# Optimization experiments

Measured on AMD Instinct MI355X. Metric: run time of the kernel, lower is better.

The kernel has to match this reference:

```python
import jax, jax.numpy as jnp
import numpy as np

B, T, D = 2, 2048, 1024
QH, KVH = 16, 4
HD = D // QH          # 64
G = QH // KVH         # group size 4
SCALE = HD ** -0.5


def _rope_rotate(x):
    # interleaved rotation: (x1, x2) -> (-x2, x1)
    x1 = x[..., ::2]
    x2 = x[..., 1::2]
    return jnp.stack((-x2, x1), axis=-1).reshape(x.shape)


def setup_inputs() -> dict:
    key = jax.random.key(0)
    k0, k1, k2, k3 = jax.random.split(key, 4)
    x = jax.random.normal(k0, (B, T, D), dtype=jnp.float32)
    # proper RoPE tables, shape [T, HD], each frequency repeated for the interleaved pair
    inv_freq = 1.0 / (10000.0 ** (np.arange(0, HD, 2, dtype=np.float32) / HD))
    freqs = np.arange(T, dtype=np.float32)[:, None] * inv_freq[None, :]   # [T, HD/2]
    freqs = np.repeat(freqs, 2, axis=-1)                                   # [T, HD]
    cos = jnp.asarray(np.cos(freqs), dtype=jnp.float32)
    sin = jnp.asarray(np.sin(freqs), dtype=jnp.float32)
    # glorot-uniform weights stored torch-style as [out, in]
    def glorot(k, out_d, in_d):
        lim = float(np.sqrt(6.0 / (in_d + out_d)))
        return jax.random.uniform(k, (out_d, in_d), jnp.float32, -lim, lim)
    Wq = glorot(k1, D, D)
    Wkv = glorot(k2, 2 * KVH * HD, D)
    Wo = glorot(k3, D, D)
    return {"x": x, "cos": cos, "sin": sin, "Wq": Wq, "Wkv": Wkv, "Wo": Wo}


def reference(x, cos, sin, Wq, Wkv, Wo):
    # projections (torch Linear: y = x @ W.T)
    q = (x @ Wq.T).reshape(B, T, QH, HD).transpose(0, 2, 1, 3)        # [B,QH,T,HD]
    kv = (x @ Wkv.T).reshape(B, T, KVH, 2, HD)
    k = kv[..., 0, :].transpose(0, 2, 1, 3)                            # [B,KVH,T,HD]
    v = kv[..., 1, :].transpose(0, 2, 1, 3)                            # [B,KVH,T,HD]
    # inline RoPE (cos/sin broadcast over batch & heads)
    q = q * cos + _rope_rotate(q) * sin
    k = k * cos + _rope_rotate(k) * sin
    # GQA via broadcast instead of repeat_interleave (same math)
    qg = q.reshape(B, KVH, G, T, HD)
    scores = jnp.einsum('bkgtd,bksd->bkgts', qg, k) * SCALE            # [B,KVH,G,T,T]
    attn = jax.nn.softmax(scores, axis=-1)  # dropout is identity in eval
    out = jnp.einsum('bkgts,bksd->bkgtd', attn, v)                     # [B,KVH,G,T,HD]
    out = out.reshape(B, QH, T, HD).transpose(0, 2, 1, 3).reshape(B, T, D)
    return out @ Wo.T
```

## Files before the change

kernel.cpp:

```cpp
#include <hip/hip_runtime.h>


typedef __bf16 bf16x8 __attribute__((ext_vector_type(8)));
typedef float f32x4 __attribute__((ext_vector_type(4)));
typedef float f32x16 __attribute__((ext_vector_type(16)));
typedef int i32x4 __attribute__((ext_vector_type(4)));
typedef unsigned short ushort4v __attribute__((ext_vector_type(4)));
typedef unsigned short ushort8v __attribute__((ext_vector_type(8)));
typedef unsigned short u16;
typedef unsigned int u32;

#define DEVINL __device__ __forceinline__

DEVINL float bf2f(u16 u) {
  unsigned int x = ((unsigned int)u) << 16;
  return __builtin_bit_cast(float, x);
}
DEVINL u16 f2bf(float f) {
  unsigned int x = __builtin_bit_cast(unsigned int, f);
  x += 0x7fffu + ((x >> 16) & 1u);
  return (u16)(x >> 16);
}
DEVINL float exp2r(float x) {
  float r;
  asm("v_exp_f32 %0, %1" : "=v"(r) : "v"(x));
  return r;
}

constexpr int Bb = 2, Tt = 2048, Dd = 1024, QH = 16, KVH = 4, HD = 64;
constexpr float SCALE_L2E = 0.125f * 1.44269504088896340736f;
constexpr int KVSZ = 131072;

__global__ void cvt_all(const float* __restrict__ x, const float* __restrict__ Wq,
                        const float* __restrict__ Wkv, const float* __restrict__ Wo,
                        u16* __restrict__ xb, u16* __restrict__ wqkv,
                        u16* __restrict__ wob) {
  int i = blockIdx.x * 256 + threadIdx.x;
  const float* src;
  u16* dst;
  if (i < 1048576) {
    src = x; dst = xb;
  } else if (i < 1310720) {
    src = Wq - (size_t)1048576 * 4; dst = wqkv - (size_t)1048576 * 4;
  } else if (i < 1441792) {
    src = Wkv - (size_t)1310720 * 4; dst = wqkv + (size_t)1024 * 1024 - (size_t)1310720 * 4;
  } else {
    src = Wo - (size_t)1441792 * 4; dst = wob - (size_t)1441792 * 4;
  }
  float4 v = reinterpret_cast<const float4*>(src)[i];
  ushort4v o = {f2bf(v.x), f2bf(v.y), f2bf(v.z), f2bf(v.w)};
  *reinterpret_cast<ushort4v*>(dst + (size_t)i * 4) = o;
}

template <bool OUT_F32, int BNF>
__global__ __launch_bounds__(256) void gemm_bt(const u16* __restrict__ A,
                                               const u16* __restrict__ Bw,
                                               void* __restrict__ Cout, int M, int N, int K) {
  __shared__ alignas(16) u16 lA[128 * 64];
  __shared__ alignas(16) u16 lB[BNF * 32 * 64];
  const int tid = threadIdx.x;
  const int w = tid >> 6, lane = tid & 63;
  const int r16 = lane & 15, g4 = lane >> 4;
  const int row0 = blockIdx.y * 128, col0 = blockIdx.x * (BNF * 32);
  const int sr = tid >> 3, sc = tid & 7;
  const int NT = K >> 6;

  bf16x8 ra[4], rb[BNF];
  f32x4 acc[4][BNF];
#pragma unroll
  for (int i = 0; i < 4; ++i)
#pragma unroll
    for (int j = 0; j < BNF; ++j) acc[i][j] = f32x4{0.f, 0.f, 0.f, 0.f};

  const int wm = (w >> 1) * 64, wn = (w & 1) * (BNF * 8);

#pragma unroll
  for (int i = 0; i < 4; ++i) {
    int r = i * 32 + sr;
    ra[i] = *reinterpret_cast<const bf16x8*>(A + (size_t)(row0 + r) * K + sc * 8);
  }
#pragma unroll
  for (int i = 0; i < BNF; ++i) {
    int r = i * 32 + sr;
    rb[i] = *reinterpret_cast<const bf16x8*>(Bw + (size_t)(col0 + r) * K + sc * 8);
  }

  for (int kt = 0; kt < NT; ++kt) {
    __syncthreads();
#pragma unroll
    for (int i = 0; i < 4; ++i) {
      int r = i * 32 + sr;
      int c = (sc ^ (r & 7)) * 8;
      *reinterpret_cast<bf16x8*>(&lA[r * 64 + c]) = ra[i];
    }
#pragma unroll
    for (int i = 0; i < BNF; ++i) {
      int r = i * 32 + sr;
      int c = (sc ^ (r & 7)) * 8;
      *reinterpret_cast<bf16x8*>(&lB[r * 64 + c]) = rb[i];
    }
    __syncthreads();
    if (kt + 1 < NT) {
      int k0 = (kt + 1) << 6;
#pragma unroll
      for (int i = 0; i < 4; ++i) {
        int r = i * 32 + sr;
        ra[i] = *reinterpret_cast<const bf16x8*>(A + (size_t)(row0 + r) * K + k0 + sc * 8);
      }
#pragma unroll
      for (int i = 0; i < BNF; ++i) {
        int r = i * 32 + sr;
        rb[i] = *reinterpret_cast<const bf16x8*>(Bw + (size_t)(col0 + r) * K + k0 + sc * 8);
      }
    }
#pragma unroll
    for (int kk = 0; kk < 2; ++kk) {
      bf16x8 af[4], bfr[BNF];
#pragma unroll
      for (int mf = 0; mf < 4; ++mf) {
        int r = wm + mf * 16 + r16;
        int c = ((kk * 4 + g4) ^ (r & 7)) * 8;
        af[mf] = *reinterpret_cast<const bf16x8*>(&lA[r * 64 + c]);
      }
#pragma unroll
      for (int nf = 0; nf < BNF; ++nf) {
        int r = wn * 2 + nf * 16 + r16;
        int c = ((kk * 4 + g4) ^ (r & 7)) * 8;
        bfr[nf] = *reinterpret_cast<const bf16x8*>(&lB[r * 64 + c]);
      }
#pragma unroll
      for (int mf = 0; mf < 4; ++mf)
#pragma unroll
        for (int nf = 0; nf < BNF; ++nf)
          acc[mf][nf] =
              __builtin_amdgcn_mfma_f32_16x16x32_bf16(af[mf], bfr[nf], acc[mf][nf], 0, 0, 0);
    }
  }

#pragma unroll
  for (int mf = 0; mf < 4; ++mf)
#pragma unroll
    for (int nf = 0; nf < BNF; ++nf)
#pragma unroll
      for (int r = 0; r < 4; ++r) {
        size_t row = (size_t)(row0 + wm + mf * 16 + g4 * 4 + r);
        size_t col = (size_t)(col0 + wn * 2 + nf * 16 + r16);
        float v = acc[mf][nf][r];
        if (OUT_F32)
          reinterpret_cast<float*>(Cout)[row * N + col] = v;
        else
          reinterpret_cast<u16*>(Cout)[row * N + col] = f2bf(v);
      }
}

__global__ void rope_vt(const u16* __restrict__ P, const float* __restrict__ cosT,
                        const float* __restrict__ sinT, u16* __restrict__ Q,
                        u16* __restrict__ Kc, u16* __restrict__ Vf) {
  __shared__ u16 tile[64][72];
  const int bid = blockIdx.x;
  const int tid = threadIdx.x;
  if (bid < 10240) {
    int idx = bid * 256 + tid;
    int row = idx / 640, p = idx - row * 640;
    int b = row >> 11, t = row & 2047;
    int n, d;
    u16* outp;
    float scl;
    if (p < 512) {
      n = p * 2;
      int h = n >> 6;
      d = n & 63;
      outp = Q + ((size_t)(b * QH + h) * Tt + t) * HD + d;
      scl = SCALE_L2E;
    } else {
      int r2 = p - 512;
      int kvh = r2 >> 5, dp = r2 & 31;
      d = dp * 2;
      n = 1024 + kvh * 128 + d;
      int bh = b * KVH + kvh;
      int kf = d >> 4, h8 = (d >> 3) & 1, j = d & 7;
      outp = Kc + (size_t)bh * KVSZ + ((t >> 5) * 4 + kf) * 512 + (h8 * 32 + (t & 31)) * 8 + j;
      scl = 1.0f;
    }
    unsigned int pv = *reinterpret_cast<const unsigned int*>(P + (size_t)row * 1536 + n);
    float v0 = bf2f((u16)(pv & 0xffffu)), v1 = bf2f((u16)(pv >> 16));
    float c = cosT[t * HD + d], s = sinT[t * HD + d];
    float o0 = (v0 * c - v1 * s) * scl;
    float o1 = (v1 * c + v0 * s) * scl;
    unsigned int ob = (unsigned int)f2bf(o0) | ((unsigned int)f2bf(o1) << 16);
    *reinterpret_cast<unsigned int*>(outp) = ob;
  } else {
    int rem = bid - 10240;
    int bh = rem >> 5, tt = rem & 31;
    int b = bh >> 2, kvh = bh & 3;
    int t0 = tt * 64;
    int colbase = 1024 + kvh * 128 + 64;
#pragma unroll
    for (int j = 0; j < 4; ++j) {
      int rr = j * 16 + (tid >> 4);
      int cc = (tid & 15) * 4;
      *reinterpret_cast<uint2*>(&tile[rr][cc]) =
          *reinterpret_cast<const uint2*>(P + (size_t)(b * Tt + t0 + rr) * 1536 + colbase + cc);
    }
    __syncthreads();
#pragma unroll
    for (int kk = 0; kk < 2; ++kk) {
      int CH = kk * 256 + tid;
      int df = CH >> 8, sbks = (CH >> 6) & 3, h8 = (CH >> 5) & 1, l = CH & 31;
      int d = df * 32 + l;
      int c = (sbks >> 1) * 4 + (sbks & 1) * 2 + h8;
      ushort8v v;
#pragma unroll
      for (int j = 0; j < 8; ++j) v[j] = tile[c * 8 + j][d];
      u16* dst = Vf + (size_t)bh * KVSZ + (((t0 >> 6) * 2 + df) * 4 + sbks) * 512 +
                 (h8 * 32 + l) * 8;
      *reinterpret_cast<ushort8v*>(dst) = v;
    }
  }
}

__global__ __launch_bounds__(512, 4) void attn_fwd9(const u16* __restrict__ Q,
                                                    const u16* __restrict__ Kf,
                                                    const u16* __restrict__ Vf,
                                                    u16* __restrict__ Oa) {
  __shared__ alignas(16) float cmb[2][32][66];
  __shared__ alignas(16) u16 ot[2][32][72];
  const int tid = threadIdx.x;
  const int w = tid >> 6, lane = tid & 63;
  const int qsub = w & 1, spl = w >> 1;
  const int l31 = lane & 31, hi = lane >> 5;

  const int fid = blockIdx.x;
  const int xcd = fid & 7, idx = fid >> 3;
  const int b = xcd >> 2, kvh = xcd & 3;
  const int g = idx & 3, qblk = idx >> 2;
  const int h = kvh * 4 + g;
  const int t0 = qblk * 64 + qsub * 32;

  const u16* Qh = Q + ((size_t)(b * QH + h) * Tt + t0 + l31) * HD + hi * 8;
  const u16* Kp = Kf + (size_t)(b * KVH + kvh) * KVSZ + lane * 8 + (size_t)spl * 32768;
  const u16* Vp = Vf + (size_t)(b * KVH + kvh) * KVSZ + lane * 8 + (size_t)spl * 32768;

  bf16x8 qf[4];
#pragma unroll
  for (int kf = 0; kf < 4; ++kf)
    qf[kf] = *reinterpret_cast<const bf16x8*>(Qh + kf * 16);

  f32x16 oacc[2];
#pragma unroll
  for (int df = 0; df < 2; ++df)
#pragma unroll
    for (int r = 0; r < 16; ++r) oacc[df][r] = 0.f;
  float lp = 0.f;

  for (int it = 0; it < 8; ++it, Kp += 4096, Vp += 4096) {
    bf16x8 kfr[2][4];
#pragma unroll
    for (int sb = 0; sb < 2; ++sb)
#pragma unroll
      for (int kf = 0; kf < 4; ++kf)
        kfr[sb][kf] = *reinterpret_cast<const bf16x8*>(Kp + sb * 2048 + kf * 512);

    f32x16 sacc[2];
#pragma unroll
    for (int sb = 0; sb < 2; ++sb)
#pragma unroll
      for (int r = 0; r < 16; ++r) sacc[sb][r] = 0.f;
    __builtin_amdgcn_s_setprio(1);
#pragma unroll
    for (int sb = 0; sb < 2; ++sb)
#pragma unroll
      for (int kf = 0; kf < 4; ++kf)
        sacc[sb] = __builtin_amdgcn_mfma_f32_32x32x16_bf16(kfr[sb][kf], qf[kf], sacc[sb], 0, 0, 0);
    __builtin_amdgcn_s_setprio(0);

    bf16x8 vf[2][2][2];
#pragma unroll
    for (int df = 0; df < 2; ++df)
#pragma unroll
      for (int sb = 0; sb < 2; ++sb)
#pragma unroll
        for (int ks = 0; ks < 2; ++ks)
          vf[df][sb][ks] =
              *reinterpret_cast<const bf16x8*>(Vp + (size_t)(df * 4 + sb * 2 + ks) * 512);

    float a0 = 0.f, a1 = 0.f, a2 = 0.f, a3 = 0.f;
#pragma unroll
    for (int sb = 0; sb < 2; ++sb)
#pragma unroll
      for (int r = 0; r < 16; r += 4) {
        float e0 = exp2r(sacc[sb][r]);
        float e1 = exp2r(sacc[sb][r + 1]);
        float e2 = exp2r(sacc[sb][r + 2]);
        float e3 = exp2r(sacc[sb][r + 3]);
        sacc[sb][r] = e0; sacc[sb][r + 1] = e1; sacc[sb][r + 2] = e2; sacc[sb][r + 3] = e3;
        a0 += e0; a1 += e1; a2 += e2; a3 += e3;
      }
    lp += (a0 + a1) + (a2 + a3);

    bf16x8 pf[2][2];
#pragma unroll
    for (int sb = 0; sb < 2; ++sb) {
      u32 pw[8];
#pragma unroll
      for (int r2 = 0; r2 < 8; ++r2) {
        u32 o;
        asm("v_cvt_pk_bf16_f32 %0, %1, %2"
            : "=v"(o)
            : "v"(sacc[sb][2 * r2]), "v"(sacc[sb][2 * r2 + 1]));
        pw[r2] = o;
      }
      u32 fw[2][4];
#pragma unroll
      for (int pp = 0; pp < 4; ++pp) {
        int ks = pp >> 1, o = pp & 1;
        u32 a = pw[ks * 4 + o], bq = pw[ks * 4 + o + 2];
        asm("v_permlane32_swap_b32 %0, %1" : "+v"(a), "+v"(bq));
        fw[ks][o] = a;
        fw[ks][o + 2] = bq;
      }
#pragma unroll
      for (int ks = 0; ks < 2; ++ks) {
        i32x4 iv = {(int)fw[ks][0], (int)fw[ks][1], (int)fw[ks][2], (int)fw[ks][3]};
        pf[sb][ks] = __builtin_bit_cast(bf16x8, iv);
      }
    }

    __builtin_amdgcn_s_setprio(1);
#pragma unroll
    for (int df = 0; df < 2; ++df)
#pragma unroll
      for (int sb = 0; sb < 2; ++sb)
#pragma unroll
        for (int ks = 0; ks < 2; ++ks)
          oacc[df] =
              __builtin_amdgcn_mfma_f32_32x32x16_bf16(vf[df][sb][ks], pf[sb][ks], oacc[df], 0, 0, 0);
    __builtin_amdgcn_s_setprio(0);
  }

  lp += __shfl_xor(lp, 32);

  for (int src = 1; src < 4; ++src) {
    if (spl == src) {
      float* cb = &cmb[qsub][l31][0];
#pragma unroll
      for (int df = 0; df < 2; ++df)
#pragma unroll
        for (int r = 0; r < 16; ++r) {
          int d = df * 32 + (r & 3) + 8 * (r >> 2) + 4 * hi;
          cb[d] = oacc[df][r];
        }
      if (hi == 0) cb[64] = lp;
    }
    __syncthreads();
    if (spl == 0) {
      const float* cb = &cmb[qsub][l31][0];
      lp += cb[64];
#pragma unroll
      for (int df = 0; df < 2; ++df)
#pragma unroll
        for (int r = 0; r < 16; ++r) {
          int d = df * 32 + (r & 3) + 8 * (r >> 2) + 4 * hi;
          oacc[df][r] += cb[d];
        }
    }
    __syncthreads();
  }

  if (spl == 0) {
    float linv = 1.0f / lp;
#pragma unroll
    for (int df = 0; df < 2; ++df)
#pragma unroll
      for (int r = 0; r < 16; ++r) {
        int d = df * 32 + (r & 3) + 8 * (r >> 2) + 4 * hi;
        ot[qsub][l31][d] = f2bf(oacc[df][r] * linv);
      }
  }
  __syncthreads();
  if (spl == 0) {
    int tr = lane >> 1, dblk = (lane & 1) * 32;
    u16* gdst = Oa + ((size_t)(b * Tt + t0 + tr)) * Dd + h * HD + dblk;
#pragma unroll
    for (int c = 0; c < 4; ++c) {
      ushort8v vv = *reinterpret_cast<const ushort8v*>(&ot[qsub][tr][dblk + c * 8]);
      *reinterpret_cast<ushort8v*>(gdst + c * 8) = vv;
    }
  }
}

extern "C" void kernel_launch(void* const* d_in, const int* in_sizes, int n_in, void* d_out,
                              int out_size, void* d_ws, size_t ws_size, hipStream_t stream) {
  (void)in_sizes; (void)n_in; (void)out_size; (void)ws_size;
  const float* x = (const float*)d_in[0];
  const float* cosT = (const float*)d_in[1];
  const float* sinT = (const float*)d_in[2];
  const float* Wq = (const float*)d_in[3];
  const float* Wkv = (const float*)d_in[4];
  const float* Wo = (const float*)d_in[5];

  char* p = (char*)d_ws;
  u16* xb = (u16*)p;   p += (size_t)4096 * 1024 * 2;
  u16* wqkv = (u16*)p; p += (size_t)1536 * 1024 * 2;
  u16* wob = (u16*)p;  p += (size_t)1024 * 1024 * 2;
  u16* Pbuf = (u16*)p; p += (size_t)4096 * 1536 * 2;
  u16* Qb = (u16*)p;   p += (size_t)Bb * QH * Tt * HD * 2;
  u16* Kbuf = (u16*)p; p += (size_t)Bb * KVH * Tt * HD * 2;
  u16* Vfb = (u16*)p;  p += (size_t)Bb * KVH * HD * Tt * 2;
  u16* Ob = Pbuf;

  cvt_all<<<6656, 256, 0, stream>>>(x, Wq, Wkv, Wo, xb, wqkv, wob);
  gemm_bt<false, 4><<<dim3(12, 32), 256, 0, stream>>>(xb, wqkv, Pbuf, 4096, 1536, 1024);
  rope_vt<<<10496, 256, 0, stream>>>(Pbuf, cosT, sinT, Qb, Kbuf, Vfb);
  attn_fwd9<<<1024, 512, 0, stream>>>(Qb, Kbuf, Vfb, Ob);
  gemm_bt<true, 2><<<dim3(16, 32), 256, 0, stream>>>(Ob, wob, d_out, 4096, 1024, 1024);
}
```

Before: 107.4 us.

## Share K/V tiles across GQA heads via double-buffered LDS with async global-to-LDS loads

The attention kernel now handles all four query heads of a KV group in one block, with one wave per head per KV-split, and halves the grid. K and V tiles are staged into a double-buffered LDS arena using global_load_lds and shared by those heads, instead of each wave loading its own K/V from global memory. The KV split drops from four ways to two, so the cross-wave reduction runs once instead of three times. In exchange it adds a block-wide barrier per iteration, 64KB of LDS per block that may limit occupancy, and twice as many serial iterations per wave.

```diff
diff --git a/kernel.cpp b/kernel.cpp
--- a/kernel.cpp
+++ b/kernel.cpp
@@ -25,6 +25,11 @@
   float r;
   asm("v_exp_f32 %0, %1" : "=v"(r) : "v"(x));
   return r;
+}
+DEVINL void gld16(const u16* g, u16* l) {
+  __builtin_amdgcn_global_load_lds(
+      (const __attribute__((address_space(1))) void*)g,
+      (__attribute__((address_space(3))) void*)l, 16, 0, 0);
 }
 
 constexpr int Bb = 2, Tt = 2048, Dd = 1024, QH = 16, KVH = 4, HD = 64;
@@ -219,28 +224,29 @@
   }
 }
 
-__global__ __launch_bounds__(512, 4) void attn_fwd9(const u16* __restrict__ Q,
-                                                    const u16* __restrict__ Kf,
-                                                    const u16* __restrict__ Vf,
-                                                    u16* __restrict__ Oa) {
-  __shared__ alignas(16) float cmb[2][32][66];
-  __shared__ alignas(16) u16 ot[2][32][72];
+__global__ __launch_bounds__(512, 4) void attn_fwd10(const u16* __restrict__ Q,
+                                                     const u16* __restrict__ Kf,
+                                                     const u16* __restrict__ Vf,
+                                                     u16* __restrict__ Oa) {
+  __shared__ alignas(16) u16 arena[32768];
   const int tid = threadIdx.x;
   const int w = tid >> 6, lane = tid & 63;
-  const int qsub = w & 1, spl = w >> 1;
+  const int g = w & 3, spl = w >> 2;
   const int l31 = lane & 31, hi = lane >> 5;
 
   const int fid = blockIdx.x;
   const int xcd = fid & 7, idx = fid >> 3;
   const int b = xcd >> 2, kvh = xcd & 3;
-  const int g = idx & 3, qblk = idx >> 2;
   const int h = kvh * 4 + g;
-  const int t0 = qblk * 64 + qsub * 32;
+  const int t0 = idx * 32;
+  const size_t bh = (size_t)(b * KVH + kvh);
+
+  const int rg = w & 3;
+  const int sv = rg & 1, isV = rg >> 1;
+  const u16* gsrc = (isV ? Vf : Kf) + bh * KVSZ + sv * 65536 + spl * 2048 + lane * 8;
+  const int ldst0 = isV * 16384 + sv * 4096 + spl * 2048;
 
   const u16* Qh = Q + ((size_t)(b * QH + h) * Tt + t0 + l31) * HD + hi * 8;
-  const u16* Kp = Kf + (size_t)(b * KVH + kvh) * KVSZ + lane * 8 + (size_t)spl * 32768;
-  const u16* Vp = Vf + (size_t)(b * KVH + kvh) * KVSZ + lane * 8 + (size_t)spl * 32768;
-
   bf16x8 qf[4];
 #pragma unroll
   for (int kf = 0; kf < 4; ++kf)
@@ -253,36 +259,36 @@
     for (int r = 0; r < 16; ++r) oacc[df][r] = 0.f;
   float lp = 0.f;
 
-  for (int it = 0; it < 8; ++it, Kp += 4096, Vp += 4096) {
-    bf16x8 kfr[2][4];
-#pragma unroll
-    for (int sb = 0; sb < 2; ++sb)
+#pragma unroll
+  for (int i = 0; i < 4; ++i) gld16(gsrc + i * 512, &arena[ldst0 + i * 512]);
+  __syncthreads();
+
+  int cur = 0;
+  for (int it = 0; it < 16; ++it) {
+    if (it < 15) {
+      const u16* gs = gsrc + (it + 1) * 4096;
+      u16* ld = &arena[ldst0 + (cur ^ 1) * 8192];
+#pragma unroll
+      for (int i = 0; i < 4; ++i) gld16(gs + i * 512, ld + i * 512);
+    }
+    const int ktb = cur * 8192 + spl * 4096;
+    const int vtb = 16384 + cur * 8192 + spl * 4096;
+
+    f32x16 sacc[2];
+#pragma unroll
+    for (int sb = 0; sb < 2; ++sb) {
+      bf16x8 kfr[4];
 #pragma unroll
       for (int kf = 0; kf < 4; ++kf)
-        kfr[sb][kf] = *reinterpret_cast<const bf16x8*>(Kp + sb * 2048 + kf * 512);
-
-    f32x16 sacc[2];
-#pragma unroll
-    for (int sb = 0; sb < 2; ++sb)
+        kfr[kf] = *reinterpret_cast<const bf16x8*>(&arena[ktb + sb * 2048 + kf * 512 + lane * 8]);
 #pragma unroll
       for (int r = 0; r < 16; ++r) sacc[sb][r] = 0.f;
-    __builtin_amdgcn_s_setprio(1);
-#pragma unroll
-    for (int sb = 0; sb < 2; ++sb)
+      __builtin_amdgcn_s_setprio(1);
 #pragma unroll
       for (int kf = 0; kf < 4; ++kf)
-        sacc[sb] = __builtin_amdgcn_mfma_f32_32x32x16_bf16(kfr[sb][kf], qf[kf], sacc[sb], 0, 0, 0);
-    __builtin_amdgcn_s_setprio(0);
-
-    bf16x8 vf[2][2][2];
-#pragma unroll
-    for (int df = 0; df < 2; ++df)
-#pragma unroll
-      for (int sb = 0; sb < 2; ++sb)
-#pragma unroll
-        for (int ks = 0; ks < 2; ++ks)
-          vf[df][sb][ks] =
-              *reinterpret_cast<const bf16x8*>(Vp + (size_t)(df * 4 + sb * 2 + ks) * 512);
+        sacc[sb] = __builtin_amdgcn_mfma_f32_32x32x16_bf16(kfr[kf], qf[kf], sacc[sb], 0, 0, 0);
+      __builtin_amdgcn_s_setprio(0);
+    }
 
     float a0 = 0.f, a1 = 0.f, a2 = 0.f, a3 = 0.f;
 #pragma unroll
@@ -332,58 +338,50 @@
 #pragma unroll
       for (int sb = 0; sb < 2; ++sb)
 #pragma unroll
-        for (int ks = 0; ks < 2; ++ks)
-          oacc[df] =
-              __builtin_amdgcn_mfma_f32_32x32x16_bf16(vf[df][sb][ks], pf[sb][ks], oacc[df], 0, 0, 0);
+        for (int ks = 0; ks < 2; ++ks) {
+          bf16x8 vfr = *reinterpret_cast<const bf16x8*>(
+              &arena[vtb + (df * 4 + sb * 2 + ks) * 512 + lane * 8]);
+          oacc[df] = __builtin_amdgcn_mfma_f32_32x32x16_bf16(vfr, pf[sb][ks], oacc[df], 0, 0, 0);
+        }
     __builtin_amdgcn_s_setprio(0);
+
+    __syncthreads();
+    cur ^= 1;
   }
 
   lp += __shfl_xor(lp, 32);
-
-  for (int src = 1; src < 4; ++src) {
-    if (spl == src) {
-      float* cb = &cmb[qsub][l31][0];
-#pragma unroll
-      for (int df = 0; df < 2; ++df)
-#pragma unroll
-        for (int r = 0; r < 16; ++r) {
-          int d = df * 32 + (r & 3) + 8 * (r >> 2) + 4 * hi;
-          cb[d] = oacc[df][r];
-        }
-      if (hi == 0) cb[64] = lp;
-    }
-    __syncthreads();
-    if (spl == 0) {
-      const float* cb = &cmb[qsub][l31][0];
-      lp += cb[64];
-#pragma unroll
-      for (int df = 0; df < 2; ++df)
-#pragma unroll
-        for (int r = 0; r < 16; ++r) {
-          int d = df * 32 + (r & 3) + 8 * (r >> 2) + 4 * hi;
-          oacc[df][r] += cb[d];
-        }
-    }
-    __syncthreads();
-  }
-
-  if (spl == 0) {
-    float linv = 1.0f / lp;
+  float* cb = reinterpret_cast<float*>(arena) + ((size_t)g * 32 + l31) * 66;
+  if (spl == 1) {
 #pragma unroll
     for (int df = 0; df < 2; ++df)
 #pragma unroll
       for (int r = 0; r < 16; ++r) {
         int d = df * 32 + (r & 3) + 8 * (r >> 2) + 4 * hi;
-        ot[qsub][l31][d] = f2bf(oacc[df][r] * linv);
-      }
+        cb[d] = oacc[df][r];
+      }
+    if (hi == 0) cb[64] = lp;
   }
   __syncthreads();
   if (spl == 0) {
+    lp += cb[64];
+    float linv = 1.0f / lp;
+    u16* otg = arena + 17408 + g * 2304;
+#pragma unroll
+    for (int df = 0; df < 2; ++df)
+#pragma unroll
+      for (int r = 0; r < 16; ++r) {
+        int d = df * 32 + (r & 3) + 8 * (r >> 2) + 4 * hi;
+        otg[l31 * 72 + d] = f2bf((oacc[df][r] + cb[d]) * linv);
+      }
+  }
+  __syncthreads();
+  if (spl == 0) {
+    const u16* otg = arena + 17408 + g * 2304;
     int tr = lane >> 1, dblk = (lane & 1) * 32;
     u16* gdst = Oa + ((size_t)(b * Tt + t0 + tr)) * Dd + h * HD + dblk;
 #pragma unroll
     for (int c = 0; c < 4; ++c) {
-      ushort8v vv = *reinterpret_cast<const ushort8v*>(&ot[qsub][tr][dblk + c * 8]);
+      ushort8v vv = *reinterpret_cast<const ushort8v*>(&otg[tr * 72 + dblk + c * 8]);
       *reinterpret_cast<ushort8v*>(gdst + c * 8) = vv;
     }
   }
@@ -412,6 +410,6 @@
   cvt_all<<<6656, 256, 0, stream>>>(x, Wq, Wkv, Wo, xb, wqkv, wob);
   gemm_bt<false, 4><<<dim3(12, 32), 256, 0, stream>>>(xb, wqkv, Pbuf, 4096, 1536, 1024);
   rope_vt<<<10496, 256, 0, stream>>>(Pbuf, cosT, sinT, Qb, Kbuf, Vfb);
-  attn_fwd9<<<1024, 512, 0, stream>>>(Qb, Kbuf, Vfb, Ob);
+  attn_fwd10<<<512, 512, 0, stream>>>(Qb, Kbuf, Vfb, Ob);
   gemm_bt<true, 2><<<dim3(16, 32), 256, 0, stream>>>(Ob, wob, d_out, 4096, 1024, 1024);
 }
```

Result: faster. 99.86 us (-7.0%).
